# Kernel tuning notes

Hardware: AMD Instinct MI355X
Metric: run time of the kernel (lower is better)

The kernel has to match this reference:

```python
import jax, jax.numpy as jnp
import numpy as np

B, IMG_ROWS, TSTEPS = 64, 32, 128
HID, CIN = 64, 512  # ncde hidden, ncde input dim = 32 * (IMG_ROWS//2)


def _linear(x, w, b):
    return x @ w.T + b


def _conv(x, w, b, pad):
    y = jax.lax.conv_general_dilated(x, w, (1, 1), [(pad, pad), (pad, pad)],
                                     dimension_numbers=('NCHW', 'OIHW', 'NCHW'))
    return y + b[None, :, None, None]


def _maxpool2(x):
    return jax.lax.reduce_window(x, -jnp.inf, jax.lax.max, (1, 1, 2, 2), (1, 1, 2, 2), 'VALID')


def _natural_cubic_coeffs(x):
    # x: [B, L, C], uniform knots t=0..L-1 (h=1). Natural cubic spline.
    L = x.shape[1]
    n = L - 2
    A = 4.0 * jnp.eye(n, dtype=x.dtype) + jnp.eye(n, k=1, dtype=x.dtype) + jnp.eye(n, k=-1, dtype=x.dtype)
    rhs = 6.0 * (x[:, 2:] - 2.0 * x[:, 1:-1] + x[:, :-2])  # [B, n, C]
    Mi = jnp.linalg.solve(A, rhs.transpose(1, 0, 2).reshape(n, -1))
    Mi = Mi.reshape(n, x.shape[0], x.shape[2]).transpose(1, 0, 2)
    M = jnp.pad(Mi, ((0, 0), (1, 1), (0, 0)))  # natural BCs: M0 = M_{L-1} = 0
    a = x[:, :-1]
    b = (x[:, 1:] - x[:, :-1]) - (2.0 * M[:, :-1] + M[:, 1:]) / 6.0
    c = M[:, :-1] / 2.0
    d = (M[:, 1:] - M[:, :-1]) / 6.0
    return a, b, c, d  # each [B, L-1, C]


def _forward(x, conv1_w, conv1_b, conv2_w, conv2_b, att_fc1_w, att_fc1_b,
             att_fc2_w, att_fc2_b, initial_w, initial_b, f1_w, f1_b,
             f2_w, f2_b, out_w, out_b):
    h = jax.nn.relu(_conv(x, conv1_w, conv1_b, pad=2))
    h = jax.nn.relu(_conv(h, conv2_w, conv2_b, pad=1))
    h = _maxpool2(h)  # [B,32,16,T/2]  (dropout is identity in eval)
    att = h.mean(axis=(2, 3))  # AdaptiveAvgPool2d(1)
    att = jax.nn.sigmoid(_linear(jax.nn.relu(_linear(att, att_fc1_w, att_fc1_b)), att_fc2_w, att_fc2_b))
    h = h * att[:, :, None, None]
    h = jnp.transpose(h, (0, 3, 1, 2))
    seq = h.reshape(h.shape[0], h.shape[1], -1)  # [B, L, 512]
    L = seq.shape[1]
    _, sb, sc, sd = _natural_cubic_coeffs(seq)

    z0 = _linear(seq[:, 0], initial_w, initial_b)  # spline.evaluate(t0) == seq[:,0]

    def cdefunc(z):
        u = jax.nn.relu(_linear(z, f1_w, f1_b))
        u = jnp.tanh(_linear(u, f2_w, f2_b))
        return u.reshape(z.shape[0], HID, CIN)

    def dXdt(t):
        seg = jnp.clip(jnp.floor(t).astype(jnp.int32), 0, L - 2)
        fr = t - seg.astype(t.dtype)
        return sb[:, seg] + 2.0 * sc[:, seg] * fr + 3.0 * sd[:, seg] * fr * fr

    def vf(t, z):
        return jnp.einsum('bhc,bc->bh', cdefunc(z), dXdt(t))

    dt = jnp.float32(0.5)
    nsteps = 2 * (L - 1)

    @jax.checkpoint
    def step(z, t):
        k1 = vf(t, z)
        k2 = vf(t + dt / 2, z + dt / 2 * k1)
        k3 = vf(t + dt / 2, z + dt / 2 * k2)
        k4 = vf(t + dt, z + dt * k3)
        return z + dt / 6.0 * (k1 + 2 * k2 + 2 * k3 + k4), None

    ts = jnp.arange(nsteps, dtype=jnp.float32) * dt
    zT, _ = jax.lax.scan(step, z0, ts)
    return _linear(zT, out_w, out_b)


def setup_inputs() -> dict:
    key = jax.random.key(0)
    ks = jax.random.split(key, 10)
    s = lambda k, shape, sc=0.05: (jax.random.normal(k, shape, jnp.float32) * sc)
    z = lambda n: jnp.zeros((n,), jnp.float32)
    return {
        'x': jax.random.normal(ks[0], (B, 1, IMG_ROWS, TSTEPS), jnp.float32),
        'conv1_w': s(ks[1], (32, 1, 5, 5)), 'conv1_b': z(32),
        'conv2_w': s(ks[2], (32, 32, 3, 3)), 'conv2_b': z(32),
        'att_fc1_w': s(ks[3], (4, 32)), 'att_fc1_b': z(4),
        'att_fc2_w': s(ks[4], (32, 4)), 'att_fc2_b': z(32),
        'initial_w': s(ks[5], (HID, CIN)), 'initial_b': z(HID),
        'f1_w': s(ks[6], (128, HID)), 'f1_b': z(128),
        'f2_w': s(ks[7], (CIN * HID, 128)), 'f2_b': z(CIN * HID),
        'out_w': s(ks[8], (2, HID)), 'out_b': z(2),
    }


def reference(x, conv1_w, conv1_b, conv2_w, conv2_b, att_fc1_w, att_fc1_b,
              att_fc2_w, att_fc2_b, initial_w, initial_b, f1_w, f1_b,
              f2_w, f2_b, out_w, out_b):
    return _forward(x, conv1_w, conv1_b, conv2_w, conv2_b, att_fc1_w, att_fc1_b,
                    att_fc2_w, att_fc2_b, initial_w, initial_b, f1_w, f1_b,
                    f2_w, f2_b, out_w, out_b)
```

## Files before the change

### kernel.cpp

```cpp
#include <hip/hip_runtime.h>
#include <hip/hip_bf16.h>
#include <stdint.h>

#define NSTEP 126
#define NEVAL 504
#define POISON 0xAAAAAAAAu

typedef __bf16 v8bf __attribute__((ext_vector_type(8)));
typedef float  v4f  __attribute__((ext_vector_type(4)));

__device__ __forceinline__ unsigned short f2bf(float x) {
  union { float f; uint32_t u; } v; v.f = x;
  uint32_t u = v.u;
  uint32_t r = (u + 0x7FFFu + ((u >> 16) & 1u)) >> 16;
  return (unsigned short)r;
}
__device__ __forceinline__ float bf2f(unsigned short b) {
  union { uint32_t u; float f; } v; v.u = ((uint32_t)b) << 16;
  return v.f;
}
__device__ __forceinline__ uint32_t cvt_pk_bf16(float lo, float hi) {
  uint32_t r;
  asm("v_cvt_pk_bf16_f32 %0, %1, %2" : "=v"(r) : "v"(lo), "v"(hi));
  return r;
}

#define LDA(p) __hip_atomic_load((p), __ATOMIC_RELAXED, __HIP_MEMORY_SCOPE_AGENT)

__device__ __forceinline__ uint32_t poll_rest(const uint32_t* p, uint32_t a) {
  uint32_t b = LDA(p);
  do { a = b; b = LDA(p); } while (a == POISON);
  return a;
}

#define BARL() asm volatile("s_waitcnt lgkmcnt(0)\n\ts_barrier" ::: "memory")

__global__ void k_detect(const uint32_t* __restrict__ xw, int* flag) {
  __shared__ int cnt;
  if (threadIdx.x == 0) cnt = 0;
  __syncthreads();
  uint32_t w = xw[threadIdx.x];
  int e = (int)((w >> 7) & 0xFF);
  int good = ((e >= 100) && (e <= 144)) || ((w & 0xFFFFu) == 0u);
  atomicAdd(&cnt, good);
  __syncthreads();
  if (threadIdx.x == 0) *flag = (cnt >= 192) ? 1 : 0;
}

#define NCVT 15
struct CvtArgs {
  const void* src[NCVT];
  int dstoff[NCVT];
  int len[NCVT];
  int kind[NCVT];
  int total;
};
__global__ void k_convert(CvtArgs a, float* __restrict__ ws, const int* __restrict__ flag) {
  int f = *flag;
  for (int i = blockIdx.x*256 + threadIdx.x; i < a.total; i += gridDim.x*256) {
    int t = 0; int rem = i;
    while (rem >= a.len[t]) { rem -= a.len[t]; t++; }
    float v = f ? bf2f(((const unsigned short*)a.src[t])[rem])
                : ((const float*)a.src[t])[rem];
    int d;
    if (a.kind[t] == 1) { int h = rem >> 9, c = rem & 511; d = a.dstoff[t] + c*64 + h; }
    else if (a.kind[t] == 2) {
      int co = rem / 288, r2 = rem % 288;
      int ci = r2 / 9, tt = r2 % 9;
      d = a.dstoff[t] + (co >> 4)*4608 + (ci*16 + (co & 15))*9 + tt;
    }
    else d = a.dstoff[t] + rem;
    ws[d] = v;
  }
}

__global__ void k_wbf16(const void* __restrict__ w2src, const void* __restrict__ w1src,
                        unsigned short* __restrict__ w2bf, unsigned short* __restrict__ w1bf,
                        const int* __restrict__ flag) {
  int f = *flag;
  const long N2 = 4194304, N1 = 8192;
  for (long i = (long)blockIdx.x*256 + threadIdx.x; i < N2 + N1; i += (long)gridDim.x*256) {
    if (i < N2) w2bf[i] = f ? ((const unsigned short*)w2src)[i] : f2bf(((const float*)w2src)[i]);
    else { long j = i - N2; w1bf[j] = f ? ((const unsigned short*)w1src)[j] : f2bf(((const float*)w1src)[j]); }
  }
}

__global__ void k_conv1(const float* __restrict__ xf, const float* __restrict__ w,
                        const float* __restrict__ bias, float* __restrict__ h1) {
  int x = threadIdx.x;
  int y = blockIdx.x;
  int b = blockIdx.y;
  const float* xin = xf + (long)b*4096;
  float in[25];
  #pragma unroll
  for (int ky = 0; ky < 5; ky++) {
    int yy = y + ky - 2;
    #pragma unroll
    for (int kx = 0; kx < 5; kx++) {
      int xx = x + kx - 2;
      in[ky*5+kx] = (yy >= 0 && yy < 32 && xx >= 0 && xx < 128) ? xin[yy*128 + xx] : 0.f;
    }
  }
  for (int co = 0; co < 32; co++) {
    float acc = bias[co];
    #pragma unroll
    for (int t = 0; t < 25; t++) acc += in[t] * w[co*25 + t];
    h1[(((long)b*32 + co)*32 + y)*128 + x] = fmaxf(acc, 0.f);
  }
}

#define LD2 132
__global__ __launch_bounds__(256) void k_conv2(const float* __restrict__ h1, const float* __restrict__ w,
                                               const float* __restrict__ bias, float* __restrict__ h2) {
  __shared__ float s[32][3][LD2];
  int y = blockIdx.x, b = blockIdx.y;
  int tid = threadIdx.x;
  for (int i = tid; i < 32*3*LD2; i += 256) {
    int ci = i / (3*LD2);
    int r  = (i / LD2) % 3;
    int xx = i % LD2;
    int yy = y + r - 1, sx = xx - 1;
    float v = 0.f;
    if (yy >= 0 && yy < 32 && sx >= 0 && sx < 128) v = h1[(((long)b*32+ci)*32+yy)*128+sx];
    s[ci][r][xx] = v;
  }
  __syncthreads();
  int x = tid & 127;
  int half = __builtin_amdgcn_readfirstlane(tid >> 7);
  const float* wb = w + half*4608;
  float acc[16];
  #pragma unroll
  for (int i = 0; i < 16; i++) acc[i] = bias[half*16 + i];
  #pragma unroll 2
  for (int ci = 0; ci < 32; ci++) {
    float xv[9];
    #pragma unroll
    for (int r = 0; r < 3; r++)
      #pragma unroll
      for (int k = 0; k < 3; k++) xv[r*3+k] = s[ci][r][x + k];
    #pragma unroll
    for (int co = 0; co < 16; co++) {
      const float* wr = wb + (ci*16 + co)*9;
      #pragma unroll
      for (int t = 0; t < 9; t++) acc[co] += xv[t] * wr[t];
    }
  }
  #pragma unroll
  for (int co = 0; co < 16; co++)
    h2[(((long)b*32 + half*16 + co)*32 + y)*128 + x] = fmaxf(acc[co], 0.f);
}

__global__ void k_pool(const float* __restrict__ h2, float* __restrict__ pooled, float* __restrict__ attm) {
  int bc = blockIdx.x;
  const float* src = h2 + (long)bc*4096;
  float* dst = pooled + (long)bc*1024;
  float sum = 0.f;
  for (int i = threadIdx.x; i < 1024; i += 256) {
    int py = i >> 6, px = i & 63;
    const float* p = src + py*256 + px*2;
    float m = fmaxf(fmaxf(p[0], p[1]), fmaxf(p[128], p[129]));
    dst[i] = m;
    sum += m;
  }
  __shared__ float red[256];
  red[threadIdx.x] = sum;
  __syncthreads();
  for (int s2 = 128; s2 > 0; s2 >>= 1) {
    if (threadIdx.x < s2) red[threadIdx.x] += red[threadIdx.x + s2];
    __syncthreads();
  }
  if (threadIdx.x == 0) attm[bc] = red[0] * (1.f/1024.f);
}

__global__ void k_att(const float* __restrict__ attm, const float* __restrict__ w1, const float* __restrict__ b1,
                      const float* __restrict__ w2, const float* __restrict__ b2, float* __restrict__ atts) {
  int b = threadIdx.x;
  if (b < 64) {
    float hb[4];
    #pragma unroll
    for (int j = 0; j < 4; j++) {
      float s = b1[j];
      for (int i = 0; i < 32; i++) s += attm[b*32+i]*w1[j*32+i];
      hb[j] = fmaxf(s, 0.f);
    }
    for (int o = 0; o < 32; o++) {
      float s = b2[o];
      #pragma unroll
      for (int j = 0; j < 4; j++) s += hb[j]*w2[o*4+j];
      atts[b*32+o] = 1.f/(1.f + __expf(-s));
    }
  }
}

__global__ void k_seq(const float* __restrict__ pooled, const float* __restrict__ atts, float* __restrict__ seq) {
  for (int idx = blockIdx.x*256 + threadIdx.x; idx < 64*64*512; idx += gridDim.x*256) {
    int b = idx >> 15;
    int t = (idx >> 9) & 63;
    int fch = idx & 511;
    int c = fch >> 4, hh = fch & 15;
    seq[idx] = pooled[(((long)b*32 + c)*16 + hh)*64 + t] * atts[b*32 + c];
  }
}

__global__ __launch_bounds__(256, 1) void k_spline(const float* __restrict__ seq,
                                                   float* __restrict__ dxt) {
  int id = blockIdx.x*256 + threadIdx.x;
  int b = id >> 9, f = id & 511;
  const float* xp = seq + (long)b*32768 + f;
  float xv[64];
  #pragma unroll
  for (int t = 0; t < 64; t++) xv[t] = xp[t*512];
  float cp[62], dp[62];
  float pc = 0.f, pd = 0.f;
  #pragma unroll
  for (int i = 0; i < 62; i++) {
    float rhs = 6.f*(xv[i+2] - 2.f*xv[i+1] + xv[i]);
    float inv = 1.f/(4.f - pc);
    pc = inv;
    pd = (rhs - pd)*inv;
    cp[i] = pc; dp[i] = pd;
  }
  #pragma unroll
  for (int i = 60; i >= 0; i--) dp[i] = dp[i] - cp[i]*dp[i+1];
  const float i6 = 1.f/6.f;
  float* op = dxt + (long)b*512 + f;
  #pragma unroll
  for (int t = 0; t < 63; t++) {
    float M0 = (t == 0)  ? 0.f : dp[t-1];
    float M1 = (t == 62) ? 0.f : dp[t];
    float sb = (xv[t+1] - xv[t]) - (2.f*M0 + M1)*i6;
    float sc = 0.5f*M0;
    float sd = (M1 - M0)*i6;
    float* o = op + (long)(4*t)*32768;
    o[0]      = sb;
    o[32768]  = sb + 0.5f*sc + 0.1875f*sd;
    o[65536]  = sb + sc + 0.75f*sd;
    o[98304]  = sb + 1.5f*sc + 1.6875f*sd;
    if (t == 62) o[131072] = sb + 2.f*sc + 3.f*sd;
  }
}

__global__ void k_z0(const float* __restrict__ seq, const float* __restrict__ iwT,
                     const float* __restrict__ ib, float* __restrict__ z0) {
  __shared__ float s0[512];
  int b = blockIdx.x, h = threadIdx.x;
  for (int c = h; c < 512; c += 64) s0[c] = seq[(long)b*32768 + c];
  __syncthreads();
  float acc = ib[h];
  for (int c = 0; c < 512; c++) acc += s0[c]*iwT[c*64 + h];
  z0[b*64 + h] = acc;
}

__global__ __launch_bounds__(512, 2) void k_ode(
    const float* __restrict__ z0buf,
    const unsigned short* __restrict__ w2bf,
    const unsigned short* __restrict__ w1bf,
    const float* __restrict__ f1bias,
    const float* __restrict__ f2bias,
    const float* __restrict__ dxt,
    const float* __restrict__ outw,
    const float* __restrict__ outb,
    uint32_t* kpart,
    void* dout,
    const int* __restrict__ flag)
{
  __shared__ __align__(16) unsigned short zs[16*72];
  __shared__ __align__(16) unsigned short ub[16*136];
  __shared__ __align__(16) float dxs[16*524 + 10560];
  __shared__ float kred[128];

  int tid = threadIdx.x;
  int bl  = blockIdx.x;
  int hb  = bl >> 2;
  int bq  = bl & 3;
  int B0  = bq*16;
  int lane = tid & 63, wv = tid >> 6;
  int q = lane >> 4, ln = lane & 15;

  v8bf w2f[4][4];
  #pragma unroll
  for (int jt = 0; jt < 4; jt++)
    #pragma unroll
    for (int ks = 0; ks < 4; ks++) {
      long row = (long)hb*512 + wv*64 + jt*16 + ln;
      w2f[jt][ks] = *(const v8bf*)(w2bf + row*128 + ks*32 + q*8);
    }
  v8bf w1f[2];
  #pragma unroll
  for (int ks = 0; ks < 2; ks++)
    w1f[ks] = *(const v8bf*)(w1bf + (wv*16 + ln)*64 + ks*32 + q*8);
  float fb2[4][4];
  #pragma unroll
  for (int jt = 0; jt < 4; jt++)
    #pragma unroll
    for (int r = 0; r < 4; r++)
      fb2[jt][r] = f2bias[(long)hb*512 + wv*64 + jt*16 + q*4 + r];
  float fb1[4];
  #pragma unroll
  for (int r = 0; r < 4; r++)
    fb1[r] = f1bias[wv*16 + q*4 + r];

  int zbL = tid & 15;
  int hg  = tid >> 4;
  int h0  = hg*2;
  float z[2], zacc[2];
  #pragma unroll
  for (int i = 0; i < 2; i++) { z[i] = z0buf[(B0+zbL)*64 + h0 + i]; zacc[i] = 0.f; }

  v4f dxc[4];
  const float dt6 = 0.5f/6.f;
  int e = 0;
  for (int step = 0; step < NSTEP; step++) {
    #pragma unroll 1
    for (int stage = 0; stage < 4; stage++, e++) {
      bool do_dx = (stage == 1) || (stage == 3) || (e == 0);
      int m = 2*step + ((stage + 1) >> 1);
      if (do_dx) {
        const float* dxb = dxt + (long)m*32768 + (B0+ln)*512 + wv*64 + q*4;
        #pragma unroll
        for (int jt = 0; jt < 4; jt++)
          dxc[jt] = *(const v4f*)(dxb + jt*16);
      }
      if (e > 0) {
        const uint32_t* kp = kpart + ((long)(e-1)*4 + bq)*1024;
        const uint32_t* p0 = kp + (h0+0)*16 + zbL;
        const uint32_t* p1 = kp + (h0+1)*16 + zbL;
        uint32_t kvu0 = LDA(p0);
        uint32_t kvu1 = LDA(p1);
        if (__builtin_expect(kvu0 == POISON, 0)) kvu0 = poll_rest(p0, kvu0);
        if (__builtin_expect(kvu1 == POISON, 0)) kvu1 = poll_rest(p1, kvu1);
        float kv0 = __uint_as_float(kvu0);
        float kv1 = __uint_as_float(kvu1);
        if (stage == 0) {
          z[0] += dt6*(zacc[0] + kv0);
          z[1] += dt6*(zacc[1] + kv1);
          zacc[0] = 0.f; zacc[1] = 0.f;
          *(uint32_t*)(zs + zbL*72 + h0) = cvt_pk_bf16(z[0], z[1]);
        } else {
          float wk = (stage == 1) ? 1.f : 2.f;
          float aa = (stage == 3) ? 0.5f : 0.25f;
          zacc[0] += wk*kv0;
          zacc[1] += wk*kv1;
          *(uint32_t*)(zs + zbL*72 + h0) = cvt_pk_bf16(z[0] + aa*kv0, z[1] + aa*kv1);
        }
      } else {
        *(uint32_t*)(zs + zbL*72 + h0) = cvt_pk_bf16(z[0], z[1]);
      }
      BARL();
      v8bf zf[2];
      #pragma unroll
      for (int ks = 0; ks < 2; ks++)
        zf[ks] = *(const v8bf*)(zs + ln*72 + ks*32 + q*8);
      {
        v4f ua = (v4f){fb1[0], fb1[1], fb1[2], fb1[3]};
        #pragma unroll
        for (int ks = 0; ks < 2; ks++)
          ua = __builtin_amdgcn_mfma_f32_16x16x32_bf16(w1f[ks], zf[ks], ua, 0, 0, 0);
        uint2 upk;
        upk.x = cvt_pk_bf16(fmaxf(ua[0], 0.f), fmaxf(ua[1], 0.f));
        upk.y = cvt_pk_bf16(fmaxf(ua[2], 0.f), fmaxf(ua[3], 0.f));
        *(uint2*)(ub + ln*136 + wv*16 + q*4) = upk;
      }
      BARL();
      v8bf uf[4];
      #pragma unroll
      for (int ks = 0; ks < 4; ks++)
        uf[ks] = *(const v8bf*)(ub + ln*136 + ks*32 + q*8);
      float ksum = 0.f;
      #pragma unroll
      for (int jt = 0; jt < 4; jt++) {
        v4f acc = (v4f){fb2[jt][0], fb2[jt][1], fb2[jt][2], fb2[jt][3]};
        #pragma unroll
        for (int ks = 0; ks < 4; ks++)
          acc = __builtin_amdgcn_mfma_f32_16x16x32_bf16(w2f[jt][ks], uf[ks], acc, 0, 0, 0);
        v4f dx4 = dxc[jt];
        #pragma unroll
        for (int r = 0; r < 4; r++) {
          float xv2 = acc[r];
          float ex = __expf(2.f*xv2);
          float th = 1.f - 2.f*__builtin_amdgcn_rcpf(ex + 1.f);
          ksum += th*dx4[r];
        }
      }
      ksum += __shfl_xor(ksum, 16, 64);
      ksum += __shfl_xor(ksum, 32, 64);
      if (lane < 16)
        kred[ln*8 + wv] = ksum;
      BARL();
      if (tid < 16) {
        const float* kr = kred + tid*8;
        float v = ((((((kr[0]+kr[1])+kr[2])+kr[3])+kr[4])+kr[5])+kr[6])+kr[7];
        uint32_t uv = __float_as_uint(v);
        if (uv == POISON) uv ^= 1u;
        __hip_atomic_store(kpart + (((long)e*4 + bq)*64 + hb)*16 + tid, uv,
                           __ATOMIC_RELAXED, __HIP_MEMORY_SCOPE_AGENT);
      }
    }
  }
  if (hb == 0) {
    const uint32_t* kp = kpart + ((long)(NEVAL-1)*4 + bq)*1024;
    {
      #pragma unroll
      for (int i = 0; i < 2; i++) {
        const uint32_t* p = kp + (h0+i)*16 + zbL;
        uint32_t v = LDA(p);
        if (v == POISON) v = poll_rest(p, v);
        z[i] += dt6*(zacc[i] + __uint_as_float(v));
      }
    }
    float o0 = z[0]*outw[h0] + z[1]*outw[h0+1];
    float o1 = z[0]*outw[64+h0] + z[1]*outw[64+h0+1];
    __syncthreads();
    dxs[hg*32 + zbL*2 + 0] = o0;
    dxs[hg*32 + zbL*2 + 1] = o1;
    __syncthreads();
    if (tid < 32) {
      int bloc = tid >> 1, comp = tid & 1;
      float s = outb[comp];
      #pragma unroll
      for (int g = 0; g < 32; g++) s += dxs[g*32 + bloc*2 + comp];
      int b = B0 + bloc;
      if (*flag) ((unsigned short*)dout)[b*2 + comp] = f2bf(s);
      else       ((float*)dout)[b*2 + comp] = s;
    }
  }
}

extern "C" void kernel_launch(void* const* d_in, const int* in_sizes, int n_in,
                              void* d_out, int out_size, void* d_ws, size_t ws_size,
                              hipStream_t stream) {
  (void)in_sizes; (void)n_in; (void)out_size; (void)ws_size;
  float* ws = (float*)d_ws;
  size_t o = 0;
  auto alloc = [&](size_t n) { size_t r = o; o += (n + 63) & ~(size_t)63; return r; };
  size_t o_flag = alloc(64);
  size_t o_xf   = alloc(262144);
  size_t o_c1w  = alloc(800);
  size_t o_c1b  = alloc(32);
  size_t o_c2w  = alloc(9216);
  size_t o_c2b  = alloc(32);
  size_t o_a1w  = alloc(128);
  size_t o_a1b  = alloc(4);
  size_t o_a2w  = alloc(128);
  size_t o_a2b  = alloc(32);
  size_t o_iwT  = alloc(32768);
  size_t o_ib   = alloc(64);
  size_t o_f1b  = alloc(128);
  size_t o_f2b  = alloc(32768);
  size_t o_ow   = alloc(128);
  size_t o_ob   = alloc(2);
  size_t o_z0   = alloc(4096);
  size_t o_attm = alloc(2048);
  size_t o_atts = alloc(2048);
  size_t o_w1bf = alloc(4096);
  size_t o_w2bf = alloc(2097152);
  size_t o_h1   = alloc(8388608);
  size_t o_h2   = alloc(8388608);
  size_t o_kpart= alloc(4128768);
  size_t o_pool = o_h1;
  size_t o_seq  = o_h1 + 2097152;
  size_t o_dxt  = o_h2;

  int* flag = (int*)(ws + o_flag);

  hipLaunchKernelGGL(k_detect, dim3(1), dim3(256), 0, stream, (const uint32_t*)d_in[0], flag);

  CvtArgs ca;
  const int  si[NCVT]  = {0,1,2,3,4,5,6,7,8,9,10,12,14,15,16};
  const size_t dofs[NCVT] = {o_xf,o_c1w,o_c1b,o_c2w,o_c2b,o_a1w,o_a1b,o_a2w,o_a2b,o_iwT,o_ib,o_f1b,o_f2b,o_ow,o_ob};
  const int  ln[NCVT]  = {262144,800,32,9216,32,128,4,128,32,32768,64,128,32768,128,2};
  int tot = 0;
  for (int i = 0; i < NCVT; i++) {
    ca.src[i] = d_in[si[i]];
    ca.dstoff[i] = (int)dofs[i];
    ca.len[i] = ln[i];
    ca.kind[i] = (si[i] == 9) ? 1 : ((si[i] == 3) ? 2 : 0);
    tot += ln[i];
  }
  ca.total = tot;
  hipLaunchKernelGGL(k_convert, dim3(512), dim3(256), 0, stream, ca, ws, flag);
  hipLaunchKernelGGL(k_wbf16, dim3(2048), dim3(256), 0, stream, d_in[13], d_in[11],
                     (unsigned short*)(ws + o_w2bf), (unsigned short*)(ws + o_w1bf), flag);
  hipLaunchKernelGGL(k_conv1, dim3(32,64), dim3(128), 0, stream, ws+o_xf, ws+o_c1w, ws+o_c1b, ws+o_h1);
  hipLaunchKernelGGL(k_conv2, dim3(32,64), dim3(256), 0, stream, ws+o_h1, ws+o_c2w, ws+o_c2b, ws+o_h2);
  hipLaunchKernelGGL(k_pool, dim3(2048), dim3(256), 0, stream, ws+o_h2, ws+o_pool, ws+o_attm);
  hipLaunchKernelGGL(k_att, dim3(1), dim3(64), 0, stream, ws+o_attm, ws+o_a1w, ws+o_a1b, ws+o_a2w, ws+o_a2b, ws+o_atts);
  hipLaunchKernelGGL(k_seq, dim3(2048), dim3(256), 0, stream, ws+o_pool, ws+o_atts, ws+o_seq);
  hipLaunchKernelGGL(k_spline, dim3(128), dim3(256), 0, stream, ws+o_seq, ws+o_dxt);
  hipLaunchKernelGGL(k_z0, dim3(64), dim3(64), 0, stream, ws+o_seq, ws+o_iwT, ws+o_ib, ws+o_z0);

  hipLaunchKernelGGL(k_ode, dim3(256), dim3(512), 0, stream,
                     ws + o_z0,
                     (const unsigned short*)(ws + o_w2bf),
                     (const unsigned short*)(ws + o_w1bf),
                     ws + o_f1b, ws + o_f2b,
                     ws + o_dxt, ws + o_ow, ws + o_ob,
                     (uint32_t*)(ws + o_kpart),
                     d_out, (const int*)flag);
}
```

Before: 1.462 ms.

## Split ODE output columns across twice as many blocks with two-part reduction

Each block of the persistent ODE kernel now covers half of its f2 output rows, selected by a new `ch` index, and the grid doubles to 512 blocks. Consumers read two partial k-values per hidden unit from a kpart buffer twice the previous size and add them. Polling now sleeps between retries. A large unused shared array is shrunk so more blocks can fit per CU. The aim is to shorten the serial per-stage MFMA and tanh work and spread it over more CUs. The cost is twice the cross-block flag traffic, plus a dependence on the workspace and its poison initialisation being sized for the larger kpart.

```diff
diff --git a/kernel.cpp b/kernel.cpp
--- a/kernel.cpp
+++ b/kernel.cpp
@@ -26,12 +26,6 @@
 }
 
 #define LDA(p) __hip_atomic_load((p), __ATOMIC_RELAXED, __HIP_MEMORY_SCOPE_AGENT)
-
-__device__ __forceinline__ uint32_t poll_rest(const uint32_t* p, uint32_t a) {
-  uint32_t b = LDA(p);
-  do { a = b; b = LDA(p); } while (a == POISON);
-  return a;
-}
 
 #define BARL() asm volatile("s_waitcnt lgkmcnt(0)\n\ts_barrier" ::: "memory")
 
@@ -251,7 +245,7 @@
   z0[b*64 + h] = acc;
 }
 
-__global__ __launch_bounds__(512, 2) void k_ode(
+__global__ __launch_bounds__(512, 4) void k_ode(
     const float* __restrict__ z0buf,
     const unsigned short* __restrict__ w2bf,
     const unsigned short* __restrict__ w1bf,
@@ -266,35 +260,37 @@
 {
   __shared__ __align__(16) unsigned short zs[16*72];
   __shared__ __align__(16) unsigned short ub[16*136];
-  __shared__ __align__(16) float dxs[16*524 + 10560];
+  __shared__ __align__(16) float po[1056];
   __shared__ float kred[128];
 
   int tid = threadIdx.x;
   int bl  = blockIdx.x;
-  int hb  = bl >> 2;
-  int bq  = bl & 3;
+  int hb  = (bl >> 3) & 63;
+  int sub = (bl + (bl >> 8)) & 7;
+  int bq  = sub & 3;
+  int ch  = sub >> 2;
   int B0  = bq*16;
   int lane = tid & 63, wv = tid >> 6;
   int q = lane >> 4, ln = lane & 15;
 
-  v8bf w2f[4][4];
-  #pragma unroll
-  for (int jt = 0; jt < 4; jt++)
+  v8bf w2f[2][4];
+  #pragma unroll
+  for (int jt = 0; jt < 2; jt++)
     #pragma unroll
     for (int ks = 0; ks < 4; ks++) {
-      long row = (long)hb*512 + wv*64 + jt*16 + ln;
+      long row = (long)hb*512 + ch*256 + wv*32 + jt*16 + ln;
       w2f[jt][ks] = *(const v8bf*)(w2bf + row*128 + ks*32 + q*8);
     }
   v8bf w1f[2];
   #pragma unroll
   for (int ks = 0; ks < 2; ks++)
     w1f[ks] = *(const v8bf*)(w1bf + (wv*16 + ln)*64 + ks*32 + q*8);
-  float fb2[4][4];
-  #pragma unroll
-  for (int jt = 0; jt < 4; jt++)
+  float fb2[2][4];
+  #pragma unroll
+  for (int jt = 0; jt < 2; jt++)
     #pragma unroll
     for (int r = 0; r < 4; r++)
-      fb2[jt][r] = f2bias[(long)hb*512 + wv*64 + jt*16 + q*4 + r];
+      fb2[jt][r] = f2bias[(long)hb*512 + ch*256 + wv*32 + jt*16 + q*4 + r];
   float fb1[4];
   #pragma unroll
   for (int r = 0; r < 4; r++)
@@ -307,7 +303,7 @@
   #pragma unroll
   for (int i = 0; i < 2; i++) { z[i] = z0buf[(B0+zbL)*64 + h0 + i]; zacc[i] = 0.f; }
 
-  v4f dxc[4];
+  v4f dxc[2];
   const float dt6 = 0.5f/6.f;
   int e = 0;
   for (int step = 0; step < NSTEP; step++) {
@@ -316,21 +312,23 @@
       bool do_dx = (stage == 1) || (stage == 3) || (e == 0);
       int m = 2*step + ((stage + 1) >> 1);
       if (do_dx) {
-        const float* dxb = dxt + (long)m*32768 + (B0+ln)*512 + wv*64 + q*4;
-        #pragma unroll
-        for (int jt = 0; jt < 4; jt++)
-          dxc[jt] = *(const v4f*)(dxb + jt*16);
+        const float* dxb = dxt + (long)m*32768 + (B0+ln)*512 + ch*256 + wv*32 + q*4;
+        dxc[0] = *(const v4f*)(dxb);
+        dxc[1] = *(const v4f*)(dxb + 16);
       }
       if (e > 0) {
-        const uint32_t* kp = kpart + ((long)(e-1)*4 + bq)*1024;
-        const uint32_t* p0 = kp + (h0+0)*16 + zbL;
-        const uint32_t* p1 = kp + (h0+1)*16 + zbL;
-        uint32_t kvu0 = LDA(p0);
-        uint32_t kvu1 = LDA(p1);
-        if (__builtin_expect(kvu0 == POISON, 0)) kvu0 = poll_rest(p0, kvu0);
-        if (__builtin_expect(kvu1 == POISON, 0)) kvu1 = poll_rest(p1, kvu1);
-        float kv0 = __uint_as_float(kvu0);
-        float kv1 = __uint_as_float(kvu1);
+        const uint32_t* kp = kpart + ((long)(e-1)*4 + bq)*2048;
+        const uint32_t* pA0 = kp + (h0+0)*16 + zbL;
+        const uint32_t* pA1 = kp + (h0+1)*16 + zbL;
+        const uint32_t* pB0 = kp + 1024 + (h0+0)*16 + zbL;
+        const uint32_t* pB1 = kp + 1024 + (h0+1)*16 + zbL;
+        uint32_t a0 = LDA(pA0), a1 = LDA(pA1), b0 = LDA(pB0), b1 = LDA(pB1);
+        while (a0 == POISON) { __builtin_amdgcn_s_sleep(1); a0 = LDA(pA0); }
+        while (a1 == POISON) { __builtin_amdgcn_s_sleep(1); a1 = LDA(pA1); }
+        while (b0 == POISON) { __builtin_amdgcn_s_sleep(1); b0 = LDA(pB0); }
+        while (b1 == POISON) { __builtin_amdgcn_s_sleep(1); b1 = LDA(pB1); }
+        float kv0 = __uint_as_float(a0) + __uint_as_float(b0);
+        float kv1 = __uint_as_float(a1) + __uint_as_float(b1);
         if (stage == 0) {
           z[0] += dt6*(zacc[0] + kv0);
           z[1] += dt6*(zacc[1] + kv1);
@@ -368,7 +366,7 @@
         uf[ks] = *(const v8bf*)(ub + ln*136 + ks*32 + q*8);
       float ksum = 0.f;
       #pragma unroll
-      for (int jt = 0; jt < 4; jt++) {
+      for (int jt = 0; jt < 2; jt++) {
         v4f acc = (v4f){fb2[jt][0], fb2[jt][1], fb2[jt][2], fb2[jt][3]};
         #pragma unroll
         for (int ks = 0; ks < 4; ks++)
@@ -392,33 +390,33 @@
         float v = ((((((kr[0]+kr[1])+kr[2])+kr[3])+kr[4])+kr[5])+kr[6])+kr[7];
         uint32_t uv = __float_as_uint(v);
         if (uv == POISON) uv ^= 1u;
-        __hip_atomic_store(kpart + (((long)e*4 + bq)*64 + hb)*16 + tid, uv,
+        __hip_atomic_store(kpart + ((((long)e*4 + bq)*2 + ch)*64 + hb)*16 + tid, uv,
                            __ATOMIC_RELAXED, __HIP_MEMORY_SCOPE_AGENT);
       }
     }
   }
-  if (hb == 0) {
-    const uint32_t* kp = kpart + ((long)(NEVAL-1)*4 + bq)*1024;
-    {
-      #pragma unroll
-      for (int i = 0; i < 2; i++) {
-        const uint32_t* p = kp + (h0+i)*16 + zbL;
-        uint32_t v = LDA(p);
-        if (v == POISON) v = poll_rest(p, v);
-        z[i] += dt6*(zacc[i] + __uint_as_float(v));
-      }
+  if (hb == 0 && ch == 0) {
+    const uint32_t* kp = kpart + ((long)(NEVAL-1)*4 + bq)*2048;
+    #pragma unroll
+    for (int i = 0; i < 2; i++) {
+      const uint32_t* pa = kp + (h0+i)*16 + zbL;
+      const uint32_t* pb = kp + 1024 + (h0+i)*16 + zbL;
+      uint32_t va = LDA(pa), vb = LDA(pb);
+      while (va == POISON) { __builtin_amdgcn_s_sleep(1); va = LDA(pa); }
+      while (vb == POISON) { __builtin_amdgcn_s_sleep(1); vb = LDA(pb); }
+      z[i] += dt6*(zacc[i] + (__uint_as_float(va) + __uint_as_float(vb)));
     }
     float o0 = z[0]*outw[h0] + z[1]*outw[h0+1];
     float o1 = z[0]*outw[64+h0] + z[1]*outw[64+h0+1];
     __syncthreads();
-    dxs[hg*32 + zbL*2 + 0] = o0;
-    dxs[hg*32 + zbL*2 + 1] = o1;
+    po[hg*32 + zbL*2 + 0] = o0;
+    po[hg*32 + zbL*2 + 1] = o1;
     __syncthreads();
     if (tid < 32) {
       int bloc = tid >> 1, comp = tid & 1;
       float s = outb[comp];
       #pragma unroll
-      for (int g = 0; g < 32; g++) s += dxs[g*32 + bloc*2 + comp];
+      for (int g = 0; g < 32; g++) s += po[g*32 + bloc*2 + comp];
       int b = B0 + bloc;
       if (*flag) ((unsigned short*)dout)[b*2 + comp] = f2bf(s);
       else       ((float*)dout)[b*2 + comp] = s;
@@ -489,7 +487,7 @@
   hipLaunchKernelGGL(k_spline, dim3(128), dim3(256), 0, stream, ws+o_seq, ws+o_dxt);
   hipLaunchKernelGGL(k_z0, dim3(64), dim3(64), 0, stream, ws+o_seq, ws+o_iwT, ws+o_ib, ws+o_z0);
 
-  hipLaunchKernelGGL(k_ode, dim3(256), dim3(512), 0, stream,
+  hipLaunchKernelGGL(k_ode, dim3(512), dim3(512), 0, stream,
                      ws + o_z0,
                      (const unsigned short*)(ws + o_w2bf),
                      (const unsigned short*)(ws + o_w1bf),
```

Result: slower. 2.142 ms (+46.5%).
